# Kernel optimization log

Measured on AMD Instinct MI355X. Metric: run time of the kernel, lower is better.

The kernel has to match this reference:

```python
import jax, jax.numpy as jnp
import numpy as np
from jax import lax

PATCH = 15
WIDTH_DCP = 55


def _box_sum(x, r):
    # AvgPool2d(kernel=2r+1, stride=1, padding=r, count_include_pad=True) * (2r+1)^2;
    # the kernel-size factor cancels in all mean_*/N ratios below.
    return lax.reduce_window(x, 0.0, lax.add, (1, 1, 2 * r + 1, 2 * r + 1),
                             (1, 1, 1, 1), ((0, 0), (0, 0), (r, r), (r, r)))


def _guided_filter(I, p, r, eps):
    Nn = _box_sum(jnp.ones_like(p), r)
    mean_I = _box_sum(I, r) / Nn
    mean_p = _box_sum(p, r) / Nn
    mean_Ip = _box_sum(I * p, r) / Nn
    cov_Ip = mean_Ip - mean_I * mean_p
    mean_II = _box_sum(I * I, r) / Nn
    var_I = mean_II - mean_I * mean_I
    a = cov_Ip / (var_I + eps)
    b = mean_p - a * mean_I
    mean_a = _box_sum(a, r) / Nn
    mean_b = _box_sum(b, r) / Nn
    return mean_a * I + mean_b


def _dark_channel(x):
    d = x.min(axis=1, keepdims=True)
    pad = WIDTH_DCP // 2
    d = jnp.pad(d, ((0, 0), (0, 0), (pad, pad), (pad, pad)), constant_values=1.0)
    return lax.reduce_window(d, jnp.inf, lax.min, (1, 1, WIDTH_DCP, WIDTH_DCP),
                             (1, 1, 1, 1), 'VALID')


def _map_A(x):
    N, C, H, W = x.shape
    dc = _dark_channel(x).reshape(N, -1)
    k = int(H * W * 0.001)
    _, idx = lax.top_k(dc, k)  # brightest dark-channel pixels
    xr = x.reshape(N, 3, -1)
    searched = jnp.take_along_axis(xr, jnp.broadcast_to(idx[:, None, :], (N, 3, k)), axis=2)
    A = searched.mean(axis=2)
    return jnp.broadcast_to(A[:, :, None, None], x.shape)


def _t_bccr(haze, mapA, ps):
    t1 = (mapA - haze) / (mapA - 20.0 / 255.0)
    t2 = (mapA - haze) / (mapA - 300.0 / 255.0)
    t = jnp.maximum(t1, t2).max(axis=1, keepdims=True)
    pad = ps // 2
    t = jnp.pad(t, ((0, 0), (0, 0), (pad, pad), (pad, pad)), constant_values=0.0)
    t = lax.reduce_window(t, -jnp.inf, lax.max, (1, 1, ps, ps), (1, 1, 1, 1), 'VALID')
    return jnp.clip(t, 0.05, 1.0)


def _pad_reshape(data, ps):
    N, C, H, W = data.shape
    pad_H = (ps - H % ps) % ps
    pad_W = (ps - W % ps) % ps
    padded = jnp.pad(data, ((0, 0), (0, 0), (pad_H // 2, pad_H - pad_H // 2),
                            (pad_W // 2, pad_W - pad_W // 2)), mode='edge')
    nH = padded.shape[2] // ps
    nW = padded.shape[3] // ps
    p = padded[:, 0].reshape(N, nH, ps, nW, ps).transpose(0, 1, 3, 2, 4)
    p = p.reshape(N, nH * nW, ps * ps).transpose(0, 2, 1)  # [N, ps*ps, P]
    return p, pad_H // 2, pad_W // 2, nH, nW


def _transmission(S, V1, ps, pixel_number=10, slp_length=0.1):
    X, sH, sW, nH, nW = _pad_reshape(V1, ps)  # [N, pp, P]
    Y, _, _, _, _ = _pad_reshape(S, ps)
    dX = X[:, :, None, :] - X[:, None, :, :]          # [N, pp, pp, P]
    dY = Y[:, :, None, :] - Y[:, None, :, :]
    slope = dY / (dX + 1e-8)
    smask = ((slope > -1) & (slope < 0)).astype(X.dtype)
    scount = smask.sum(axis=2)                         # [N, pp, P]
    pmask = (scount >= 0.5 * ps * ps).astype(X.dtype)
    pcount = pmask.sum(axis=1, keepdims=True)          # [N, 1, P]
    mx = (X * pmask).sum(axis=1, keepdims=True) / (pcount + 1e-5)
    my = (Y * pmask).sum(axis=1, keepdims=True) / (pcount + 1e-5)
    k = ((X * Y * pmask).sum(axis=1, keepdims=True) - pcount * mx * my) / (
        ((X * pmask) ** 2).sum(axis=1, keepdims=True) - pcount * mx ** 2 + 1e-5)
    b = my - k * mx
    t = 1.0 + k / (b + 1e-8)
    length = (1.0 + k ** 2) ** 0.5 * ((X * pmask).max(axis=1, keepdims=True)
                                      - (X + 1e8 * (1.0 - pmask)).min(axis=1, keepdims=True))
    tmask = ((pcount > pixel_number) & (length > slp_length) & (k > -1) & (k < 0)
             & (t > 0.01) & (t < 1 - 0.01)).astype(X.dtype)
    t = (t * tmask).reshape(-1, 1, nH, nW)
    t = jnp.repeat(jnp.repeat(t, ps, axis=2), ps, axis=3)  # nearest upsample x ps
    return t[:, :, sH:S.shape[2] + sH, sW:S.shape[3] + sW]


def _percentile(t, bili=0.05):
    N = t.shape[0]
    flat = jnp.where(t > 0, t, 10.0).reshape(N, -1)
    s = jnp.sort(flat, axis=1)
    n = flat.shape[1]
    idx = min(int(bili * n), n - 1)
    return s[:, idx].reshape(-1, 1, 1, 1)


def _restore(image, ps=PATCH):
    mapA = _map_A(image)
    norm = image / mapA
    mx = norm.max(axis=1, keepdims=True)
    S = 1.0 - norm.min(axis=1, keepdims=True) / (mx + 1e-8)
    V1 = 1.0 / (mx + 1e-8)
    t1 = _transmission(S, V1, ps)
    half = ps // 2
    t2 = _transmission(S[:, :, half:, half:], V1[:, :, half:, half:], ps)
    t2 = jnp.pad(t2, ((0, 0), (0, 0), (half, 0), (half, 0)), constant_values=0.0)
    t_slp = jnp.where((t1 != 0) & (t2 != 0), (t1 + t2) / 2.0,
                      jnp.where(t1 != 0, t1, t2))
    t_bl = _t_bccr(image, mapA, ps)
    t_min = _percentile(t_slp)
    t_fusion = jnp.clip(jnp.where(t_slp > 0, t_slp, t_bl), t_min, 1.0)
    t_ref = _guided_filter(image.mean(axis=1, keepdims=True), t_fusion, 2 * ps, 1e-3)
    return (image - mapA) / t_ref + mapA


def setup_inputs() -> dict:
    key = jax.random.key(0)
    image = jax.random.uniform(key, (1, 3, 480, 480), dtype=jnp.float32)
    return {"image": image}


def reference(image):
    return _restore(image)
```

## Files before the change

kernel.cpp:

```cpp
#include <hip/hip_runtime.h>
#include <math.h>

#define W 480
#define HT 480
#define HW (W*HT)
#define NT (HW/256)
#define PP 225
#define NPATCH 1024
#define EQCAP 8192

struct State {
  unsigned slotP[4];
  unsigned slotK[4];
  float sumA[3];
  unsigned eqCount;
  float A[3];
  unsigned tminbits;
  unsigned eqIdx[EQCAP];
  float tp1[NPATCH];
  float tp2[NPATCH];
};

__device__ __forceinline__ void resolve_level(const unsigned* __restrict__ h,
                                              unsigned k_in, int desc,
                                              unsigned* lds,
                                              unsigned& chosen, unsigned& k_out) {
  int t = threadIdx.x;
  unsigned c = h[desc ? (255 - t) : t];
  lds[t] = c;
  __syncthreads();
  for (int s = 1; s < 256; s <<= 1) {
    unsigned add = (t >= s) ? lds[t - s] : 0u;
    __syncthreads();
    lds[t] += add;
    __syncthreads();
  }
  unsigned incl = lds[t];
  unsigned excl = incl - c;
  if (incl >= k_in && excl < k_in) { lds[256] = (unsigned)t; lds[257] = k_in - excl; }
  __syncthreads();
  unsigned tt = lds[256];
  k_out = lds[257];
  chosen = desc ? (255u - tt) : tt;
  __syncthreads();
}

__device__ __forceinline__ float wred_sum(float v) { for (int m = 32; m; m >>= 1) v += __shfl_xor(v, m, 64); return v; }
__device__ __forceinline__ float wred_max(float v) { for (int m = 32; m; m >>= 1) v = fmaxf(v, __shfl_xor(v, m, 64)); return v; }
__device__ __forceinline__ float wred_min(float v) { for (int m = 32; m; m >>= 1) v = fminf(v, __shfl_xor(v, m, 64)); return v; }

__global__ __launch_bounds__(512) void k_rowmin(const float* __restrict__ img,
                                                float* __restrict__ rowmin,
                                                State* st, unsigned* __restrict__ hist16) {
  __shared__ float l[534];
  int y = blockIdx.x, t = threadIdx.x;
  int g = y * 512 + t;
  if (g < 65536) hist16[g] = 0u;
  for (int i = t; i < 534; i += 512) {
    int col = i - 27;
    float v = 1.0f;
    if ((unsigned)col < (unsigned)W) {
      int q = y * W + col;
      v = fminf(fminf(img[q], img[HW + q]), img[2 * HW + q]);
    }
    l[i] = v;
  }
  if (g == 0) { st->sumA[0] = 0.f; st->sumA[1] = 0.f; st->sumA[2] = 0.f; st->eqCount = 0u; }
  __syncthreads();
  if (t < W) {
    float m = l[t];
    for (int d = 1; d < 55; ++d) m = fminf(m, l[t + d]);
    rowmin[y * W + t] = m;
  }
}

__global__ __launch_bounds__(256) void k_minV3(const float* __restrict__ rowmin,
                                               float* __restrict__ dc,
                                               unsigned* __restrict__ hist16) {
  __shared__ unsigned short bs[256];
  int t = threadIdx.x;
  int p = blockIdx.x * 256 + t;
  int y = p / W, x = p - y * W;
  int lo = y - 27, hi = y + 27;
  float m = (lo < 0 || hi >= HT) ? 1.0f : INFINITY;
  int lo2 = max(lo, 0), hi2 = min(hi, HT - 1);
  for (int yy = lo2; yy <= hi2; ++yy) m = fminf(m, rowmin[yy * W + x]);
  dc[p] = m;
  unsigned b16 = __float_as_uint(m) >> 16;
  bs[t] = (unsigned short)b16;
  __syncthreads();
  int firstIdx = 256, cnt = 0;
  for (int j = 0; j < 256; ++j) {
    if ((unsigned)bs[j] == b16) { ++cnt; if (j < firstIdx) firstIdx = j; }
  }
  if (firstIdx == t) atomicAdd(&hist16[b16], (unsigned)cnt);
}

__global__ __launch_bounds__(256) void k_resolve16(const unsigned* __restrict__ hist16,
                                                   State* st) {
  __shared__ unsigned lds[258];
  __shared__ unsigned lh[256];
  int t = threadIdx.x;
  const uint4* h4 = (const uint4*)hist16;
  unsigned s = 0;
  for (int i = 0; i < 64; ++i) { uint4 v = h4[t * 64 + i]; s += v.x + v.y + v.z + v.w; }
  lh[t] = s;
  __syncthreads();
  unsigned ct, kc;
  resolve_level(lh, 230u, 1, lds, ct, kc);
  lh[t] = hist16[ct * 256 + t];
  __syncthreads();
  unsigned b, kp;
  resolve_level(lh, kc, 1, lds, b, kp);
  if (t == 0) { st->slotP[0] = (ct << 8) | b; st->slotK[0] = kp; }
}

__global__ __launch_bounds__(256) void k_gather2(const float* __restrict__ dc,
                                                 const float* __restrict__ img, State* st) {
  __shared__ float ls[3];
  __shared__ unsigned lcnt, lbase;
  int t = threadIdx.x;
  if (t == 0) { ls[0] = 0.f; ls[1] = 0.f; ls[2] = 0.f; lcnt = 0u; }
  __syncthreads();
  int p = blockIdx.x * 256 + t;
  unsigned p16 = st->slotP[0];
  unsigned b16 = __float_as_uint(dc[p]) >> 16;
  bool eq = (b16 == p16);
  unsigned my = 0;
  if (b16 > p16) {
    atomicAdd(&ls[0], img[p]);
    atomicAdd(&ls[1], img[HW + p]);
    atomicAdd(&ls[2], img[2 * HW + p]);
  } else if (eq) {
    my = atomicAdd(&lcnt, 1u);
  }
  __syncthreads();
  if (t == 0 && lcnt) lbase = atomicAdd(&st->eqCount, lcnt);
  __syncthreads();
  if (eq) { unsigned pos = lbase + my; if (pos < (unsigned)EQCAP) st->eqIdx[pos] = (unsigned)p; }
  if (t == 0 && (ls[0] != 0.f || ls[1] != 0.f || ls[2] != 0.f)) {
    atomicAdd(&st->sumA[0], ls[0]);
    atomicAdd(&st->sumA[1], ls[1]);
    atomicAdd(&st->sumA[2], ls[2]);
  }
}

__global__ __launch_bounds__(256) void k_finalizeA2(const float* __restrict__ dc,
                                                    const float* __restrict__ img, State* st) {
  __shared__ unsigned lds[258];
  __shared__ unsigned lh[256];
  __shared__ unsigned sIdx[EQCAP];
  __shared__ unsigned short sVal[EQCAP];
  __shared__ float ssum[3];
  int t = threadIdx.x;
  unsigned k = st->slotK[0];
  unsigned ne = st->eqCount; if (ne > (unsigned)EQCAP) ne = EQCAP;
  for (int i = t; i < (int)ne; i += 256) {
    unsigned q = st->eqIdx[i];
    sIdx[i] = q;
    sVal[i] = (unsigned short)(__float_as_uint(dc[q]) & 0xFFFFu);
  }
  if (t < 3) ssum[t] = 0.f;
  __syncthreads();
  unsigned vpfx = 0u;
  for (int lev = 0; lev < 2; ++lev) {
    int s = 8 - 8 * lev;
    lh[t] = 0u;
    __syncthreads();
    for (int i = t; i < (int)ne; i += 256) {
      unsigned v = (unsigned)sVal[i];
      if (lev == 0 || (v >> 8) == (vpfx >> 8))
        atomicAdd(&lh[(v >> s) & 0xFFu], 1u);
    }
    __syncthreads();
    unsigned ch, kn;
    resolve_level(lh, k, 1, lds, ch, kn);
    vpfx |= ch << s;
    k = kn;
  }
  unsigned pfx = 0u;
  for (int lev = 0; lev < 3; ++lev) {
    int s = 16 - 8 * lev;
    lh[t] = 0u;
    __syncthreads();
    for (int i = t; i < (int)ne; i += 256) {
      if ((unsigned)sVal[i] == vpfx) {
        unsigned v = sIdx[i];
        if ((v >> (s + 8)) == (pfx >> (s + 8)))
          atomicAdd(&lh[(v >> s) & 0xFFu], 1u);
      }
    }
    __syncthreads();
    unsigned ch, kn;
    resolve_level(lh, k, 0, lds, ch, kn);
    pfx |= ch << s;
    k = kn;
  }
  float a0 = 0.f, a1 = 0.f, a2 = 0.f;
  for (int i = t; i < (int)ne; i += 256) {
    unsigned v = (unsigned)sVal[i], q = sIdx[i];
    if (v > vpfx || (v == vpfx && q <= pfx)) {
      a0 += img[q]; a1 += img[HW + q]; a2 += img[2 * HW + q];
    }
  }
  atomicAdd(&ssum[0], a0); atomicAdd(&ssum[1], a1); atomicAdd(&ssum[2], a2);
  __syncthreads();
  if (t == 0) {
    st->A[0] = (st->sumA[0] + ssum[0]) / 230.0f;
    st->A[1] = (st->sumA[1] + ssum[1]) / 230.0f;
    st->A[2] = (st->sumA[2] + ssum[2]) / 230.0f;
  }
}

#define SLPTEST(ox, oy) \
  ((((yi - (oy)) * ((xi - (ox)) + 1e-8f)) < 0.0f) && \
   (fabsf(yi - (oy)) < fabsf((xi - (ox)) + 1e-8f)) ? 1 : 0)

__global__ __launch_bounds__(256) void k_mega1(const float* __restrict__ img,
                                               float* __restrict__ mh, State* st) {
  __shared__ __align__(16) float2 XY[PP + 1];
  __shared__ float part[4][8];
  __shared__ float Tl[494];
  int b = blockIdx.x;
  int t = threadIdx.x;
  float A0 = st->A[0], A1 = st->A[1], A2 = st->A[2];
  const float c20 = (float)(20.0 / 255.0);
  const float c300 = (float)(300.0 / 255.0);
  if (b >= 2048) {
    int y = b - 2048;
    for (int i = t; i < 494; i += 256) {
      int col = i - 7;
      float v = 0.0f;
      if ((unsigned)col < (unsigned)W) {
        int q = y * W + col;
        float r = img[q], g = img[HW + q], bl = img[2 * HW + q];
        float t0 = fmaxf((A0 - r) / (A0 - c20), (A0 - r) / (A0 - c300));
        float t1 = fmaxf((A1 - g) / (A1 - c20), (A1 - g) / (A1 - c300));
        float t2 = fmaxf((A2 - bl) / (A2 - c20), (A2 - bl) / (A2 - c300));
        v = fmaxf(fmaxf(t0, t1), t2);
      }
      Tl[i] = v;
    }
    __syncthreads();
    for (int x = t; x < W; x += 256) {
      float m = -INFINITY;
      for (int d = 0; d < 15; ++d) m = fmaxf(m, Tl[x + d]);
      mh[y * W + x] = m;
    }
    return;
  }
  int mode = b >> 10;
  int pid = b & 1023;
  int ph = pid >> 5, pw = pid & 31;
  if (t < PP) {
    int r = t / 15, c = t - (t / 15) * 15;
    int y, x;
    if (mode == 0) { y = ph * 15 + r; x = pw * 15 + c; }
    else {
      y = ph * 15 + r + 4; y = (y < 7) ? 7 : ((y > 479) ? 479 : y);
      x = pw * 15 + c + 4; x = (x < 7) ? 7 : ((x > 479) ? 479 : x);
    }
    int q = y * W + x;
    float rr = img[q], gg = img[HW + q], bb = img[2 * HW + q];
    float nr = rr / A0, ng = gg / A1, nb = bb / A2;
    float mx = fmaxf(fmaxf(nr, ng), nb);
    float mn = fminf(fminf(nr, ng), nb);
    float d = mx + 1e-8f;
    XY[t] = make_float2(1.0f / d, 1.0f - mn / d);
  }
  __syncthreads();
  float xi = 0.f, yi = 0.f;
  int cnt = 0;
  if (t < PP) {
    xi = XY[t].x; yi = XY[t].y;
    const float4* XY4 = (const float4*)XY;
    int c0 = 0, c1 = 0, c2 = 0, c3 = 0;
    #pragma unroll 2
    for (int j4 = 0; j4 < 112; j4 += 4) {
      float4 a = XY4[j4 + 0];
      float4 bq = XY4[j4 + 1];
      float4 cq = XY4[j4 + 2];
      float4 dq = XY4[j4 + 3];
      c0 += SLPTEST(a.x, a.y);   c1 += SLPTEST(a.z, a.w);
      c2 += SLPTEST(bq.x, bq.y); c3 += SLPTEST(bq.z, bq.w);
      c0 += SLPTEST(cq.x, cq.y); c1 += SLPTEST(cq.z, cq.w);
      c2 += SLPTEST(dq.x, dq.y); c3 += SLPTEST(dq.z, dq.w);
    }
    { float2 o = XY[224]; c0 += SLPTEST(o.x, o.y); }
    cnt = (c0 + c1) + (c2 + c3);
  }
  float pmf = (t < PP && cnt >= 113) ? 1.0f : 0.0f;
  float xm = xi * pmf, ym = yi * pmf;
  float v0 = wred_sum(pmf);
  float v1 = wred_sum(xm);
  float v2 = wred_sum(ym);
  float v3 = wred_sum(xm * ym);
  float v4 = wred_sum(xm * xm);
  float v5 = wred_max((t < PP) ? xm : -INFINITY);
  float v6 = wred_min((t < PP) ? (xi + 1e8f * (1.0f - pmf)) : INFINITY);
  int wid = t >> 6, lane = t & 63;
  if (lane == 0) {
    part[wid][0] = v0; part[wid][1] = v1; part[wid][2] = v2; part[wid][3] = v3;
    part[wid][4] = v4; part[wid][5] = v5; part[wid][6] = v6;
  }
  __syncthreads();
  if (t == 0) {
    float pcount = 0.f, sx = 0.f, sy = 0.f, sxy = 0.f, sxx = 0.f;
    float mxX = -INFINITY, mnX = INFINITY;
    for (int w2 = 0; w2 < 4; ++w2) {
      pcount += part[w2][0]; sx += part[w2][1]; sy += part[w2][2];
      sxy += part[w2][3]; sxx += part[w2][4];
      mxX = fmaxf(mxX, part[w2][5]); mnX = fminf(mnX, part[w2][6]);
    }
    float den = pcount + 1e-5f;
    float mxv = sx / den, myv = sy / den;
    float kk = (sxy - pcount * mxv * myv) / (sxx - pcount * (mxv * mxv) + 1e-5f);
    float bb = myv - kk * mxv;
    float tt = 1.0f + kk / (bb + 1e-8f);
    float len = sqrtf(1.0f + kk * kk) * (mxX - mnX);
    bool m = (pcount > 10.0f) && (len > 0.1f) && (kk > -1.0f) && (kk < 0.0f)
             && (tt > 0.01f) && (tt < 0.99f);
    float res = tt * (m ? 1.0f : 0.0f);
    if (mode == 0) st->tp1[pid] = res; else st->tp2[pid] = res;
  }
}

__global__ __launch_bounds__(256) void k_pct(State* st) {
  __shared__ unsigned lh[256];
  __shared__ unsigned lds[258];
  __shared__ float tp1s[NPATCH], tp2s[NPATCH];
  int t = threadIdx.x;
  for (int i = t; i < NPATCH; i += 256) { tp1s[i] = st->tp1[i]; tp2s[i] = st->tp2[i]; }
  __syncthreads();
  unsigned prefix = 0u, k = 11521u;
  for (int level = 0; level < 4; ++level) {
    lh[t] = 0u;
    __syncthreads();
    unsigned mask = (level == 0) ? 0u : (0xFFFFFFFFu << (32 - 8 * level));
    int shift = 24 - 8 * level;
    for (int i = t; i < NPATCH; i += 256) {
      int ph = i >> 5, pw = i & 31;
      float a = tp1s[i];
      int rcnt[2], ridx[2], ccnt[2], cidx[2];
      if (ph == 0) { rcnt[0] = 7; ridx[0] = -1; rcnt[1] = 8; ridx[1] = 0; }
      else         { rcnt[0] = 4; ridx[0] = ph - 1; rcnt[1] = 11; ridx[1] = ph; }
      if (pw == 0) { ccnt[0] = 7; cidx[0] = -1; ccnt[1] = 8; cidx[1] = 0; }
      else         { ccnt[0] = 4; cidx[0] = pw - 1; ccnt[1] = 11; cidx[1] = pw; }
      for (int ri = 0; ri < 2; ++ri)
        for (int ci = 0; ci < 2; ++ci) {
          unsigned area = (unsigned)(rcnt[ri] * ccnt[ci]);
          float bb = 0.0f;
          if (ridx[ri] >= 0 && cidx[ci] >= 0) bb = tp2s[ridx[ri] * 32 + cidx[ci]];
          float r;
          if (a != 0.0f && bb != 0.0f) r = (a + bb) / 2.0f;
          else r = (a != 0.0f) ? a : bb;
          float u = (r > 0.0f) ? r : 10.0f;
          unsigned bits = __float_as_uint(u);
          if ((bits & mask) == prefix)
            atomicAdd(&lh[(bits >> shift) & 0xFFu], area);
        }
    }
    __syncthreads();
    unsigned ch, kn;
    resolve_level(lh, k, 0, lds, ch, kn);
    prefix |= ch << shift;
    k = kn;
  }
  if (t == 0) st->tminbits = prefix;
}

__global__ __launch_bounds__(512) void k_gf1h(const float* __restrict__ img,
                                              const float* __restrict__ mh,
                                              const State* __restrict__ st,
                                              float4* __restrict__ box4) {
  __shared__ float tp1s[NPATCH], tp2s[NPATCH];
  __shared__ float Pl[540], Il[540];
  __shared__ float tbv[480];
  int y = blockIdx.x, t = threadIdx.x;
  for (int i = t; i < NPATCH; i += 512) { tp1s[i] = st->tp1[i]; tp2s[i] = st->tp2[i]; }
  for (int x = t; x < W; x += 512) {
    float m = -INFINITY;
    for (int d = -7; d <= 7; ++d) {
      int yy = y + d;
      float v = ((unsigned)yy < (unsigned)HT) ? mh[yy * W + x] : 0.0f;
      m = fmaxf(m, v);
    }
    tbv[x] = fminf(fmaxf(m, 0.05f), 1.0f);
  }
  __syncthreads();
  float tmin = __uint_as_float(st->tminbits);
  int c1row = (y / 15) * 32;
  bool c2ok = (y >= 7);
  int c2row = c2ok ? ((y - 4) / 15) * 32 : 0;
  for (int i = t; i < 540; i += 512) {
    int col = i - 30;
    float pv = 0.0f, iv = 0.0f;
    if ((unsigned)col < (unsigned)W) {
      int q = y * W + col;
      float a = tp1s[c1row + col / 15];
      float bb = 0.0f;
      if (c2ok && col >= 7) bb = tp2s[c2row + (col - 4) / 15];
      float r;
      if (a != 0.0f && bb != 0.0f) r = (a + bb) / 2.0f;
      else r = (a != 0.0f) ? a : bb;
      float v = (r > 0.0f) ? r : tbv[col];
      v = (v < tmin) ? tmin : v;
      v = (v > 1.0f) ? 1.0f : v;
      pv = v;
      iv = ((img[q] + img[HW + q]) + img[2 * HW + q]) / 3.0f;
    }
    Pl[i] = pv; Il[i] = iv;
  }
  __syncthreads();
  if (t < W) {
    float sI = 0.f, sP = 0.f, sIp = 0.f, sII = 0.f;
    for (int d = 0; d < 61; ++d) {
      float iv = Il[t + d], pv = Pl[t + d];
      sI += iv; sP += pv; sIp += iv * pv; sII += iv * iv;
    }
    box4[y * W + t] = make_float4(sI, sP, sIp, sII);
  }
}

__global__ __launch_bounds__(512) void k_gf1vh(const float4* __restrict__ box4,
                                               float2* __restrict__ hab) {
  __shared__ float2 l[540];
  int y = blockIdx.x, t = threadIdx.x;
  float2 v = make_float2(0.f, 0.f);
  if (t < W) {
    float sI = 0.f, sP = 0.f, sIp = 0.f, sII = 0.f;
    for (int d = -30; d <= 30; ++d) {
      int yy = y + d;
      if ((unsigned)yy < (unsigned)HT) {
        float4 b = box4[yy * W + t];
        sI += b.x; sP += b.y; sIp += b.z; sII += b.w;
      }
    }
    int ny = min(y + 30, HT - 1) - max(y - 30, 0) + 1;
    int nx = min(t + 30, W - 1) - max(t - 30, 0) + 1;
    float Nn = (float)(ny * nx);
    float mI = sI / Nn, mP = sP / Nn, mIp = sIp / Nn, mII = sII / Nn;
    float cov = mIp - mI * mP;
    float var = mII - mI * mI;
    float av = cov / (var + 1e-3f);
    v = make_float2(av, mP - av * mI);
  }
  if (t < 30) { l[t] = make_float2(0.f, 0.f); l[510 + t] = make_float2(0.f, 0.f); }
  if (t < W) l[30 + t] = v;
  __syncthreads();
  if (t < W) {
    float sa = 0.f, sb = 0.f;
    for (int d = 0; d < 61; ++d) { float2 u = l[t + d]; sa += u.x; sb += u.y; }
    hab[y * W + t] = make_float2(sa, sb);
  }
}

__global__ __launch_bounds__(256) void k_gf2vfin(const float2* __restrict__ hab,
                                                 const float* __restrict__ img,
                                                 const State* __restrict__ st,
                                                 float* __restrict__ out) {
  int p = blockIdx.x * 256 + threadIdx.x;
  int y = p / W, x = p - y * W;
  float sa = 0.f, sb = 0.f;
  for (int d = -30; d <= 30; ++d) {
    int yy = y + d;
    if ((unsigned)yy < (unsigned)HT) { float2 v = hab[yy * W + x]; sa += v.x; sb += v.y; }
  }
  int ny = min(y + 30, HT - 1) - max(y - 30, 0) + 1;
  int nx = min(x + 30, W - 1) - max(x - 30, 0) + 1;
  float Nn = (float)(ny * nx);
  float r = img[p], g = img[HW + p], bl = img[2 * HW + p];
  float Iv = ((r + g) + bl) / 3.0f;
  float tref = (sa / Nn) * Iv + (sb / Nn);
  float A0 = st->A[0], A1 = st->A[1], A2 = st->A[2];
  out[p]          = (r  - A0) / tref + A0;
  out[HW + p]     = (g  - A1) / tref + A1;
  out[2 * HW + p] = (bl - A2) / tref + A2;
}

extern "C" void kernel_launch(void* const* d_in, const int* in_sizes, int n_in,
                              void* d_out, int out_size, void* d_ws, size_t ws_size,
                              hipStream_t stream) {
  (void)in_sizes; (void)n_in; (void)out_size; (void)ws_size;
  const float* img = (const float*)d_in[0];
  float* out = (float*)d_out;
  State* st = (State*)d_ws;
  unsigned* hist16 = (unsigned*)((char*)d_ws + 65536);
  float* sb = (float*)((char*)d_ws + 65536 + 262144);
  float* bufA = sb;
  float* bufB = sb + HW;
  float4* box4 = (float4*)(sb + 2 * HW);
  float2* hab  = (float2*)(sb + 6 * HW);

  dim3 b256(256), b512(512);
  dim3 ge(NT), rows(HT);

  k_rowmin<<<rows, b512, 0, stream>>>(img, bufB, st, hist16);
  k_minV3<<<ge, b256, 0, stream>>>(bufB, bufA, hist16);
  k_resolve16<<<dim3(1), b256, 0, stream>>>(hist16, st);
  k_gather2<<<ge, b256, 0, stream>>>(bufA, img, st);
  k_finalizeA2<<<dim3(1), b256, 0, stream>>>(bufA, img, st);
  k_mega1<<<dim3(2048 + HT), b256, 0, stream>>>(img, bufB, st);
  k_pct<<<dim3(1), b256, 0, stream>>>(st);
  k_gf1h<<<rows, b512, 0, stream>>>(img, bufB, st, box4);
  k_gf1vh<<<rows, b512, 0, stream>>>(box4, hab);
  k_gf2vfin<<<ge, b256, 0, stream>>>(hab, img, st, out);
}
```

Baseline: 186.9 us.

## Use wave-shuffle scan in histogram resolve, stash eq values, simplify slope test

```diff
diff --git a/kernel.cpp b/kernel.cpp
--- a/kernel.cpp
+++ b/kernel.cpp
@@ -17,6 +17,7 @@
   float A[3];
   unsigned tminbits;
   unsigned eqIdx[EQCAP];
+  unsigned short eqVal[EQCAP];
   float tp1[NPATCH];
   float tp2[NPATCH];
 };
@@ -26,22 +27,30 @@
                                               unsigned* lds,
                                               unsigned& chosen, unsigned& k_out) {
   int t = threadIdx.x;
-  unsigned c = h[desc ? (255 - t) : t];
-  lds[t] = c;
-  __syncthreads();
-  for (int s = 1; s < 256; s <<= 1) {
-    unsigned add = (t >= s) ? lds[t - s] : 0u;
-    __syncthreads();
-    lds[t] += add;
-    __syncthreads();
-  }
-  unsigned incl = lds[t];
-  unsigned excl = incl - c;
-  if (incl >= k_in && excl < k_in) { lds[256] = (unsigned)t; lds[257] = k_in - excl; }
-  __syncthreads();
-  unsigned tt = lds[256];
+  if (t < 64) {
+    int p0 = 4 * t;
+    unsigned c0 = h[desc ? (255 - (p0 + 0)) : (p0 + 0)];
+    unsigned c1 = h[desc ? (255 - (p0 + 1)) : (p0 + 1)];
+    unsigned c2 = h[desc ? (255 - (p0 + 2)) : (p0 + 2)];
+    unsigned c3 = h[desc ? (255 - (p0 + 3)) : (p0 + 3)];
+    unsigned s0 = c0, s1 = s0 + c1, s2 = s1 + c2, s3 = s2 + c3;
+    unsigned incl = s3;
+    for (int d = 1; d < 64; d <<= 1) {
+      unsigned u = __shfl_up(incl, d, 64);
+      if (t >= d) incl += u;
+    }
+    unsigned lexcl = incl - s3;
+    unsigned i0 = lexcl + s0, i1 = lexcl + s1, i2 = lexcl + s2, i3 = lexcl + s3;
+    unsigned e0 = i0 - c0, e1 = i1 - c1, e2 = i2 - c2, e3 = i3 - c3;
+    if (i0 >= k_in && e0 < k_in) { lds[256] = (unsigned)(p0 + 0); lds[257] = k_in - e0; }
+    if (i1 >= k_in && e1 < k_in) { lds[256] = (unsigned)(p0 + 1); lds[257] = k_in - e1; }
+    if (i2 >= k_in && e2 < k_in) { lds[256] = (unsigned)(p0 + 2); lds[257] = k_in - e2; }
+    if (i3 >= k_in && e3 < k_in) { lds[256] = (unsigned)(p0 + 3); lds[257] = k_in - e3; }
+  }
+  __syncthreads();
+  unsigned p = lds[256];
   k_out = lds[257];
-  chosen = desc ? (255u - tt) : tt;
+  chosen = desc ? (255u - p) : p;
   __syncthreads();
 }
 
@@ -124,7 +133,8 @@
   __syncthreads();
   int p = blockIdx.x * 256 + t;
   unsigned p16 = st->slotP[0];
-  unsigned b16 = __float_as_uint(dc[p]) >> 16;
+  unsigned bits = __float_as_uint(dc[p]);
+  unsigned b16 = bits >> 16;
   bool eq = (b16 == p16);
   unsigned my = 0;
   if (b16 > p16) {
@@ -137,7 +147,13 @@
   __syncthreads();
   if (t == 0 && lcnt) lbase = atomicAdd(&st->eqCount, lcnt);
   __syncthreads();
-  if (eq) { unsigned pos = lbase + my; if (pos < (unsigned)EQCAP) st->eqIdx[pos] = (unsigned)p; }
+  if (eq) {
+    unsigned pos = lbase + my;
+    if (pos < (unsigned)EQCAP) {
+      st->eqIdx[pos] = (unsigned)p;
+      st->eqVal[pos] = (unsigned short)(bits & 0xFFFFu);
+    }
+  }
   if (t == 0 && (ls[0] != 0.f || ls[1] != 0.f || ls[2] != 0.f)) {
     atomicAdd(&st->sumA[0], ls[0]);
     atomicAdd(&st->sumA[1], ls[1]);
@@ -145,8 +161,7 @@
   }
 }
 
-__global__ __launch_bounds__(256) void k_finalizeA2(const float* __restrict__ dc,
-                                                    const float* __restrict__ img, State* st) {
+__global__ __launch_bounds__(256) void k_finalizeA2(const float* __restrict__ img, State* st) {
   __shared__ unsigned lds[258];
   __shared__ unsigned lh[256];
   __shared__ unsigned sIdx[EQCAP];
@@ -156,9 +171,8 @@
   unsigned k = st->slotK[0];
   unsigned ne = st->eqCount; if (ne > (unsigned)EQCAP) ne = EQCAP;
   for (int i = t; i < (int)ne; i += 256) {
-    unsigned q = st->eqIdx[i];
-    sIdx[i] = q;
-    sVal[i] = (unsigned short)(__float_as_uint(dc[q]) & 0xFFFFu);
+    sIdx[i] = st->eqIdx[i];
+    sVal[i] = st->eqVal[i];
   }
   if (t < 3) ssum[t] = 0.f;
   __syncthreads();
@@ -212,9 +226,11 @@
   }
 }
 
-#define SLPTEST(ox, oy) \
-  ((((yi - (oy)) * ((xi - (ox)) + 1e-8f)) < 0.0f) && \
-   (fabsf(yi - (oy)) < fabsf((xi - (ox)) + 1e-8f)) ? 1 : 0)
+__device__ __forceinline__ int slptest(float xi, float yi, float ox, float oy) {
+  float dY = yi - oy;
+  float D = (xi - ox) + 1e-8f;
+  return (dY * (dY + D) < 0.0f) ? 1 : 0;
+}
 
 __global__ __launch_bounds__(256) void k_mega1(const float* __restrict__ img,
                                                float* __restrict__ mh, State* st) {
@@ -281,12 +297,12 @@
       float4 bq = XY4[j4 + 1];
       float4 cq = XY4[j4 + 2];
       float4 dq = XY4[j4 + 3];
-      c0 += SLPTEST(a.x, a.y);   c1 += SLPTEST(a.z, a.w);
-      c2 += SLPTEST(bq.x, bq.y); c3 += SLPTEST(bq.z, bq.w);
-      c0 += SLPTEST(cq.x, cq.y); c1 += SLPTEST(cq.z, cq.w);
-      c2 += SLPTEST(dq.x, dq.y); c3 += SLPTEST(dq.z, dq.w);
-    }
-    { float2 o = XY[224]; c0 += SLPTEST(o.x, o.y); }
+      c0 += slptest(xi, yi, a.x, a.y);   c1 += slptest(xi, yi, a.z, a.w);
+      c2 += slptest(xi, yi, bq.x, bq.y); c3 += slptest(xi, yi, bq.z, bq.w);
+      c0 += slptest(xi, yi, cq.x, cq.y); c1 += slptest(xi, yi, cq.z, cq.w);
+      c2 += slptest(xi, yi, dq.x, dq.y); c3 += slptest(xi, yi, dq.z, dq.w);
+    }
+    { float2 o = XY[224]; c0 += slptest(xi, yi, o.x, o.y); }
     cnt = (c0 + c1) + (c2 + c3);
   }
   float pmf = (t < PP && cnt >= 113) ? 1.0f : 0.0f;
@@ -499,7 +515,7 @@
   k_minV3<<<ge, b256, 0, stream>>>(bufB, bufA, hist16);
   k_resolve16<<<dim3(1), b256, 0, stream>>>(hist16, st);
   k_gather2<<<ge, b256, 0, stream>>>(bufA, img, st);
-  k_finalizeA2<<<dim3(1), b256, 0, stream>>>(bufA, img, st);
+  k_finalizeA2<<<dim3(1), b256, 0, stream>>>(img, st);
   k_mega1<<<dim3(2048 + HT), b256, 0, stream>>>(img, bufB, st);
   k_pct<<<dim3(1), b256, 0, stream>>>(st);
   k_gf1h<<<rows, b512, 0, stream>>>(img, bufB, st, box4);
```

After: 177.9 us. -4.8%, faster.
